# Performance work log

Measured on AMD Instinct MI355X. Metric: run time of the kernel, lower is better.

## Reference

```python
import jax, jax.numpy as jnp
import numpy as np

D_MODEL = 1024
H = 16
D_K = D_MODEL // H
WINDOW = 256
NEG = -1.0e9


def setup_inputs() -> dict:
    key = jax.random.key(0)
    ks = jax.random.split(key, 12)
    B, S = 1, 4096
    scale = 1.0 / np.sqrt(D_MODEL)
    inp = {
        'q': jax.random.normal(ks[0], (B, S, D_MODEL), dtype=jnp.float32),
        'k': jax.random.normal(ks[1], (B, S, D_MODEL), dtype=jnp.float32),
        'v': jax.random.normal(ks[2], (B, S, D_MODEL), dtype=jnp.float32),
        'w_q': jax.random.normal(ks[3], (D_MODEL, D_MODEL), dtype=jnp.float32) * scale,
        'b_q': jnp.zeros((D_MODEL,), dtype=jnp.float32),
        'w_k': jax.random.normal(ks[4], (D_MODEL, D_MODEL), dtype=jnp.float32) * scale,
        'b_k': jnp.zeros((D_MODEL,), dtype=jnp.float32),
        'w_v': jax.random.normal(ks[5], (D_MODEL, D_MODEL), dtype=jnp.float32) * scale,
        'b_v': jnp.zeros((D_MODEL,), dtype=jnp.float32),
        'w_o': jax.random.normal(ks[6], (D_MODEL, D_MODEL), dtype=jnp.float32) * scale,
        'b_o': jnp.zeros((D_MODEL,), dtype=jnp.float32),
    }
    return inp


def _local_mask(seq_len: int, window_size: int) -> jnp.ndarray:
    left = (window_size - 1) // 2
    right = window_size - 1 - left
    row = jnp.arange(seq_len)[:, None]
    col = jnp.arange(seq_len)[None, :]
    return (col >= row - left) & (col <= row + right)  # [S, S] bool


def reference(q, k, v, w_q, b_q, w_k, b_k, w_v, b_v, w_o, b_o):
    B, Sq, _ = q.shape
    Sk = k.shape[1]
    # projections (torch Linear: x @ W.T + b) -> [B, h, S, d_k]
    query = (q @ w_q.T + b_q).reshape(B, Sq, H, D_K).transpose(0, 2, 1, 3)
    key = (k @ w_k.T + b_k).reshape(B, Sk, H, D_K).transpose(0, 2, 1, 3)
    value = (v @ w_v.T + b_v).reshape(B, Sk, H, D_K).transpose(0, 2, 1, 3)

    scores = jnp.einsum('bhqd,bhkd->bhqk', query, key) / jnp.sqrt(
        jnp.asarray(D_K, dtype=query.dtype))
    if Sq == Sk:
        mask = _local_mask(Sq, WINDOW)  # [S, S]
        scores = jnp.where(mask[None, None], scores, jnp.asarray(NEG, scores.dtype))
    attn = jax.nn.softmax(scores, axis=-1)
    x = jnp.einsum('bhqk,bhkd->bhqd', attn, value)
    x = x.transpose(0, 2, 1, 3).reshape(B, Sq, D_MODEL)
    return x @ w_o.T + b_o
```

## Files before the change

kernel.cpp:

```cpp
#include <hip/hip_runtime.h>

#define SEQ 4096
#define DM 1024
#define NH 16
#define DK 64

typedef _Float16 half8 __attribute__((ext_vector_type(8)));
typedef _Float16 half4v __attribute__((ext_vector_type(4)));
typedef float f32x4 __attribute__((ext_vector_type(4)));

#define MFMA16(a, b, c) __builtin_amdgcn_mfma_f32_16x16x32_f16((a), (b), (c), 0, 0, 0)
#define GLOAD_LDS(g, l)                                                                  \
    __builtin_amdgcn_global_load_lds((const __attribute__((address_space(1))) void*)(g), \
                                     (__attribute__((address_space(3))) void*)(l), 16, 0, 0)

__device__ __forceinline__ float dpp_max16(float x) {
    x = fmaxf(x, __int_as_float(__builtin_amdgcn_update_dpp(
                     0, __float_as_int(x), 0xB1, 0xF, 0xF, true)));
    x = fmaxf(x, __int_as_float(__builtin_amdgcn_update_dpp(
                     0, __float_as_int(x), 0x4E, 0xF, 0xF, true)));
    x = fmaxf(x, __int_as_float(__builtin_amdgcn_update_dpp(
                     0, __float_as_int(x), 0x124, 0xF, 0xF, true)));
    x = fmaxf(x, __int_as_float(__builtin_amdgcn_update_dpp(
                     0, __float_as_int(x), 0x128, 0xF, 0xF, true)));
    return x;
}

__global__ void cvt_all(const float* __restrict__ q, const float* __restrict__ k,
                        const float* __restrict__ v, const float* __restrict__ wq,
                        const float* __restrict__ wk, const float* __restrict__ wv,
                        const float* __restrict__ wo, _Float16* __restrict__ qh,
                        _Float16* __restrict__ kh, _Float16* __restrict__ vh,
                        _Float16* __restrict__ wqh, _Float16* __restrict__ wkh,
                        _Float16* __restrict__ wvh, _Float16* __restrict__ woh) {
    int z = blockIdx.y;
    const float* src;
    _Float16* dst;
    int n;
    switch (z) {
    case 0: src = q;  dst = qh;  n = SEQ * DM; break;
    case 1: src = k;  dst = kh;  n = SEQ * DM; break;
    case 2: src = v;  dst = vh;  n = SEQ * DM; break;
    case 3: src = wq; dst = wqh; n = DM * DM;  break;
    case 4: src = wk; dst = wkh; n = DM * DM;  break;
    case 5: src = wv; dst = wvh; n = DM * DM;  break;
    default: src = wo; dst = woh; n = DM * DM; break;
    }
    int idx = (blockIdx.x * 256 + threadIdx.x) * 8;
    if (idx >= n) return;
    float4 f0 = *(const float4*)(src + idx);
    float4 f1 = *(const float4*)(src + idx + 4);
    half8 h;
    h[0] = (_Float16)f0.x; h[1] = (_Float16)f0.y; h[2] = (_Float16)f0.z; h[3] = (_Float16)f0.w;
    h[4] = (_Float16)f1.x; h[5] = (_Float16)f1.y; h[6] = (_Float16)f1.z; h[7] = (_Float16)f1.w;
    *(half8*)(dst + idx) = h;
}

template <int MT>
__device__ __forceinline__ void gemm_bk32_db(const _Float16* __restrict__ A,
                                             const _Float16* __restrict__ B, int m0, int n0,
                                             _Float16* As, _Float16* Bs, f32x4 (*acc)[4]) {
    constexpr int MI = MT / 32;
    constexpr int ACH = MT / 64;
    constexpr int ABUF = MT * 32;
    const int tid = threadIdx.x;
    const int wave = tid >> 6, lane = tid & 63;
    const int quad = lane >> 4, l16 = lane & 15;
    const int wr = (wave >> 1) * (MT / 2);
    const int wc = (wave & 1) * 64;
    const int srow = tid >> 2, scol = (tid & 3) * 8;

#pragma unroll
    for (int j = 0; j < ACH; ++j)
        GLOAD_LDS(A + (size_t)(m0 + j * 64 + srow) * DM + scol, As + j * 2048 + tid * 8);
#pragma unroll
    for (int j = 0; j < 2; ++j)
        GLOAD_LDS(B + (size_t)(n0 + j * 64 + srow) * DM + scol, Bs + j * 2048 + tid * 8);
    __syncthreads();

    int cur = 0;
    for (int k0 = 0; k0 < DM; k0 += 32) {
        const int nxt = cur ^ 1;
        if (k0 + 32 < DM) {
            int kc = k0 + 32 + scol;
#pragma unroll
            for (int j = 0; j < ACH; ++j)
                GLOAD_LDS(A + (size_t)(m0 + j * 64 + srow) * DM + kc,
                          As + nxt * ABUF + j * 2048 + tid * 8);
#pragma unroll
            for (int j = 0; j < 2; ++j)
                GLOAD_LDS(B + (size_t)(n0 + j * 64 + srow) * DM + kc,
                          Bs + nxt * 4096 + j * 2048 + tid * 8);
        }
        half8 af[MI], bf[4];
#pragma unroll
        for (int mi = 0; mi < MI; ++mi)
            af[mi] = *(const half8*)&As[cur * ABUF + (wr + mi * 16 + l16) * 32 + quad * 8];
#pragma unroll
        for (int ni = 0; ni < 4; ++ni)
            bf[ni] = *(const half8*)&Bs[cur * 4096 + (wc + ni * 16 + l16) * 32 + quad * 8];
#pragma unroll
        for (int mi = 0; mi < MI; ++mi)
#pragma unroll
            for (int ni = 0; ni < 4; ++ni)
                acc[mi][ni] = MFMA16(af[mi], bf[ni], acc[mi][ni]);
        __syncthreads();
        cur = nxt;
    }
}

__global__ void __launch_bounds__(256, 3) gemm_qkv(
    const _Float16* __restrict__ qh, const _Float16* __restrict__ kh,
    const _Float16* __restrict__ vh, const _Float16* __restrict__ wqh,
    const _Float16* __restrict__ wkh, const _Float16* __restrict__ wvh,
    const float* __restrict__ bq, const float* __restrict__ bk, const float* __restrict__ bv,
    _Float16* __restrict__ Qo, _Float16* __restrict__ Ko, _Float16* __restrict__ Vt) {
    __shared__ _Float16 As[2 * 128 * 32];
    __shared__ _Float16 Bs[2 * 128 * 32];
    int z = blockIdx.z;
    const _Float16 *A, *B;
    const float* bias;
    float scale;
    if (z == 0) { A = qh; B = wqh; bias = bq; scale = 0.125f; }
    else if (z == 1) { A = kh; B = wkh; bias = bk; scale = 1.0f; }
    else { A = vh; B = wvh; bias = bv; scale = 1.0f; }

    int m0 = blockIdx.x * 128;
    int n0 = blockIdx.y * 128;
    f32x4 acc[4][4] = {};
    gemm_bk32_db<128>(A, B, m0, n0, As, Bs, acc);

    const int tid = threadIdx.x;
    const int wave = tid >> 6, lane = tid & 63;
    const int quad = lane >> 4, l16 = lane & 15;
    const int wr = (wave >> 1) * 64;
    const int wc = (wave & 1) * 64;
    float bs[4];
#pragma unroll
    for (int ni = 0; ni < 4; ++ni) bs[ni] = bias[n0 + wc + ni * 16 + l16];

    if (z < 2) {
        _Float16* C = (z == 0) ? Qo : Ko;
#pragma unroll
        for (int mi = 0; mi < 4; ++mi)
#pragma unroll
            for (int ni = 0; ni < 4; ++ni) {
                int m = m0 + wr + mi * 16 + quad * 4;
                int n = n0 + wc + ni * 16 + l16;
#pragma unroll
                for (int r = 0; r < 4; ++r)
                    C[(size_t)(m + r) * DM + n] = (_Float16)((acc[mi][ni][r] + bs[ni]) * scale);
            }
    } else {
#pragma unroll
        for (int mi = 0; mi < 4; ++mi)
#pragma unroll
            for (int ni = 0; ni < 4; ++ni) {
                int m = m0 + wr + mi * 16 + quad * 4;
                int n = n0 + wc + ni * 16 + l16;
                half4v p;
#pragma unroll
                for (int r = 0; r < 4; ++r) p[r] = (_Float16)(acc[mi][ni][r] + bs[ni]);
                *(half4v*)(Vt + (size_t)n * SEQ + m) = p;
            }
    }
}

__global__ void __launch_bounds__(256, 3) gemm_out(const _Float16* __restrict__ Xh,
                                                   const _Float16* __restrict__ woh,
                                                   const float* __restrict__ bo,
                                                   float* __restrict__ out) {
    __shared__ _Float16 As[2 * 64 * 32];
    __shared__ _Float16 Bs[2 * 128 * 32];
    int m0 = blockIdx.x * 64;
    int n0 = blockIdx.y * 128;
    f32x4 acc[2][4] = {};
    gemm_bk32_db<64>(Xh, woh, m0, n0, As, Bs, acc);

    const int tid = threadIdx.x;
    const int wave = tid >> 6, lane = tid & 63;
    const int quad = lane >> 4, l16 = lane & 15;
    const int wr = (wave >> 1) * 32;
    const int wc = (wave & 1) * 64;
#pragma unroll
    for (int mi = 0; mi < 2; ++mi)
#pragma unroll
        for (int ni = 0; ni < 4; ++ni) {
            int m = m0 + wr + mi * 16 + quad * 4;
            int n = n0 + wc + ni * 16 + l16;
            float b = bo[n];
#pragma unroll
            for (int r = 0; r < 4; ++r) out[(size_t)(m + r) * DM + n] = acc[mi][ni][r] + b;
        }
}

__global__ void __launch_bounds__(256, 4) attn_kernel(const _Float16* __restrict__ Q,
                                                      const _Float16* __restrict__ K,
                                                      const _Float16* __restrict__ Vt,
                                                      _Float16* __restrict__ X) {
    __shared__ _Float16 Ks[320 * 64];
    __shared__ _Float16 Pl[4][16][40];
    int tid = threadIdx.x;
    int wave = tid >> 6, lane = tid & 63;
    int quad = lane >> 4, l16 = lane & 15;
    int h = blockIdx.y;
    int bx = ((blockIdx.x & 7) << 3) + (blockIdx.x >> 3);
    int q0b = bx * 64;
    int q0 = q0b + wave * 16;
    int kspan0 = q0b - 128;

    const _Float16* Kg = K + h * DK;
#pragma unroll
    for (int i = 0; i < 10; ++i) {
        int U = i * 256 + tid;
        int row = U >> 3, u = U & 7;
        int rg = kspan0 + row;
        rg = rg < 0 ? 0 : (rg > SEQ - 1 ? SEQ - 1 : rg);
        GLOAD_LDS(Kg + (size_t)rg * DM + ((u ^ (row & 7)) << 3), Ks + U * 8);
    }

    const _Float16* Qp = Q + (size_t)(q0 + l16) * DM + h * DK + quad * 8;
    half8 aq0 = *(const half8*)(Qp);
    half8 aq1 = *(const half8*)(Qp + 32);
    const half8 ones = {(_Float16)1, (_Float16)1, (_Float16)1, (_Float16)1,
                        (_Float16)1, (_Float16)1, (_Float16)1, (_Float16)1};

    float rowM[4], rowL[4];
    f32x4 o[4] = {};
#pragma unroll
    for (int r = 0; r < 4; ++r) { rowM[r] = -__builtin_inff(); rowL[r] = 0.f; }

    int kstart = (q0 > 127) ? ((q0 - 127) & ~31) : 0;
    int kend = q0 + 143;
    if (kend > SEQ - 1) kend = SEQ - 1;
    const int xk = l16 & 7;

    __syncthreads();

    for (int kt = kstart; kt <= kend; kt += 32) {
        int rel = kt - kspan0;
        half8 vb[4];
#pragma unroll
        for (int ni = 0; ni < 4; ++ni)
            vb[ni] = *(const half8*)(Vt + (size_t)(h * DK + ni * 16 + l16) * SEQ + kt + quad * 8);

        f32x4 s[2];
#pragma unroll
        for (int cf = 0; cf < 2; ++cf) {
            int rr = rel + cf * 16 + l16;
            half8 b0 = *(const half8*)&Ks[rr * 64 + ((quad ^ xk) << 3)];
            half8 b1 = *(const half8*)&Ks[rr * 64 + (((quad + 4) ^ xk) << 3)];
            f32x4 z = {};
            z = MFMA16(aq0, b0, z);
            z = MFMA16(aq1, b1, z);
            s[cf] = z;
        }
        const bool full = (kt >= q0 - 112) && (kt <= q0 + 97);
        float alpha[4];
#pragma unroll
        for (int r = 0; r < 4; ++r) {
            float x0 = s[0][r], x1 = s[1][r];
            if (!full) {
                int row = q0 + quad * 4 + r;
                int key0 = kt + l16, key1 = kt + 16 + l16;
                if (key0 < row - 127 || key0 > row + 128) x0 = -1e30f;
                if (key1 < row - 127 || key1 > row + 128) x1 = -1e30f;
            }
            float t = dpp_max16(fmaxf(x0, x1));
            float mnew = fmaxf(rowM[r], t);
            alpha[r] = __expf(rowM[r] - mnew);
            float p0 = __expf(x0 - mnew);
            float p1 = __expf(x1 - mnew);
            Pl[wave][quad * 4 + r][l16] = (_Float16)p0;
            Pl[wave][quad * 4 + r][l16 + 16] = (_Float16)p1;
            rowM[r] = mnew;
        }
        half8 ap = *(const half8*)&Pl[wave][l16][quad * 8];
        f32x4 ts = {};
        ts = MFMA16(ap, ones, ts);
#pragma unroll
        for (int r = 0; r < 4; ++r) rowL[r] = rowL[r] * alpha[r] + ts[r];
#pragma unroll
        for (int ni = 0; ni < 4; ++ni) {
#pragma unroll
            for (int r = 0; r < 4; ++r) o[ni][r] *= alpha[r];
            o[ni] = MFMA16(ap, vb[ni], o[ni]);
        }
    }

    float rinv[4];
#pragma unroll
    for (int r = 0; r < 4; ++r) rinv[r] = 1.0f / rowL[r];
#pragma unroll
    for (int ni = 0; ni < 4; ++ni) {
        int n = h * DK + ni * 16 + l16;
#pragma unroll
        for (int r = 0; r < 4; ++r) {
            int m = q0 + quad * 4 + r;
            X[(size_t)m * DM + n] = (_Float16)(o[ni][r] * rinv[r]);
        }
    }
}

extern "C" void kernel_launch(void* const* d_in, const int* in_sizes, int n_in, void* d_out,
                              int out_size, void* d_ws, size_t ws_size, hipStream_t stream) {
    const float* q  = (const float*)d_in[0];
    const float* k  = (const float*)d_in[1];
    const float* v  = (const float*)d_in[2];
    const float* wq = (const float*)d_in[3];
    const float* bq = (const float*)d_in[4];
    const float* wk = (const float*)d_in[5];
    const float* bk = (const float*)d_in[6];
    const float* wv = (const float*)d_in[7];
    const float* bv = (const float*)d_in[8];
    const float* wo = (const float*)d_in[9];
    const float* bo = (const float*)d_in[10];

    const size_t SZ_T = (size_t)SEQ * DM * sizeof(_Float16);
    const size_t SZ_W = (size_t)DM * DM * sizeof(_Float16);
    char* p = (char*)d_ws;
    _Float16* qh  = (_Float16*)(p);
    _Float16* kh  = (_Float16*)(p + SZ_T);
    _Float16* vh  = (_Float16*)(p + 2 * SZ_T);
    _Float16* wqh = (_Float16*)(p + 3 * SZ_T);
    _Float16* wkh = (_Float16*)(p + 3 * SZ_T + SZ_W);
    _Float16* wvh = (_Float16*)(p + 3 * SZ_T + 2 * SZ_W);
    _Float16* woh = (_Float16*)(p + 3 * SZ_T + 3 * SZ_W);
    _Float16* Qo  = (_Float16*)(p + 3 * SZ_T + 4 * SZ_W);
    _Float16* Ko  = (_Float16*)(p + 4 * SZ_T + 4 * SZ_W);
    _Float16* Vt  = (_Float16*)(p + 5 * SZ_T + 4 * SZ_W);
    _Float16* Xh  = qh;

    cvt_all<<<dim3(2048, 7), 256, 0, stream>>>(q, k, v, wq, wk, wv, wo, qh, kh, vh, wqh, wkh,
                                               wvh, woh);
    gemm_qkv<<<dim3(32, 8, 3), 256, 0, stream>>>(qh, kh, vh, wqh, wkh, wvh, bq, bk, bv, Qo, Ko,
                                                 Vt);
    attn_kernel<<<dim3(SEQ / 64, NH), 256, 0, stream>>>(Qo, Ko, Vt, Xh);
    gemm_out<<<dim3(64, 8), 256, 0, stream>>>(Xh, woh, bo, (float*)d_out);
}
```

Baseline: 205.0 us.

## Prefetch two K-stages ahead in GEMM using vmcnt-counted waits

Restructures the double-buffered GEMM mainloop so both LDS buffers are filled up front. Each iteration waits with a partial s_waitcnt vmcnt, so only the current stage's loads must land, then reads fragments to registers. After a second barrier it issues the loads for k+64 into the just-consumed buffer before running the MFMAs. This keeps one extra stage of global-to-LDS loads in flight and replaces __syncthreads with raw barriers. It relies on hand-counted vmcnt values and adds wasted wraparound loads in the last iterations.

```diff
diff --git a/kernel.cpp b/kernel.cpp
--- a/kernel.cpp
+++ b/kernel.cpp
@@ -57,9 +57,9 @@
 }
 
 template <int MT>
-__device__ __forceinline__ void gemm_bk32_db(const _Float16* __restrict__ A,
-                                             const _Float16* __restrict__ B, int m0, int n0,
-                                             _Float16* As, _Float16* Bs, f32x4 (*acc)[4]) {
+__device__ __forceinline__ void gemm_bk32_cnt(const _Float16* __restrict__ A,
+                                              const _Float16* __restrict__ B, int m0, int n0,
+                                              _Float16* As, _Float16* Bs, f32x4 (*acc)[4]) {
     constexpr int MI = MT / 32;
     constexpr int ACH = MT / 64;
     constexpr int ABUF = MT * 32;
@@ -71,41 +71,55 @@
     const int srow = tid >> 2, scol = (tid & 3) * 8;
 
 #pragma unroll
-    for (int j = 0; j < ACH; ++j)
-        GLOAD_LDS(A + (size_t)(m0 + j * 64 + srow) * DM + scol, As + j * 2048 + tid * 8);
-#pragma unroll
-    for (int j = 0; j < 2; ++j)
-        GLOAD_LDS(B + (size_t)(n0 + j * 64 + srow) * DM + scol, Bs + j * 2048 + tid * 8);
-    __syncthreads();
+    for (int s = 0; s < 2; ++s) {
+        int kc = s * 32 + scol;
+#pragma unroll
+        for (int j = 0; j < ACH; ++j)
+            GLOAD_LDS(A + (size_t)(m0 + j * 64 + srow) * DM + kc,
+                      As + s * ABUF + j * 2048 + tid * 8);
+#pragma unroll
+        for (int j = 0; j < 2; ++j)
+            GLOAD_LDS(B + (size_t)(n0 + j * 64 + srow) * DM + kc,
+                      Bs + s * 4096 + j * 2048 + tid * 8);
+    }
 
     int cur = 0;
     for (int k0 = 0; k0 < DM; k0 += 32) {
-        const int nxt = cur ^ 1;
-        if (k0 + 32 < DM) {
-            int kc = k0 + 32 + scol;
+        if constexpr (MT == 128) asm volatile("s_waitcnt vmcnt(4)" ::: "memory");
+        else                     asm volatile("s_waitcnt vmcnt(3)" ::: "memory");
+        asm volatile("s_barrier" ::: "memory");
+
+        half8 af[MI], bf[4];
+#pragma unroll
+        for (int mi = 0; mi < MI; ++mi)
+            af[mi] = *(const half8*)&As[cur * ABUF + (wr + mi * 16 + l16) * 32 + quad * 8];
+#pragma unroll
+        for (int ni = 0; ni < 4; ++ni)
+            bf[ni] = *(const half8*)&Bs[cur * 4096 + (wc + ni * 16 + l16) * 32 + quad * 8];
+
+        asm volatile("s_waitcnt lgkmcnt(0)" ::: "memory");
+        __builtin_amdgcn_sched_barrier(0);
+        asm volatile("s_barrier" ::: "memory");
+
+        {
+            int k2 = k0 + 64;
+            if (k2 >= DM) k2 = 0;
+            int kc = k2 + scol;
 #pragma unroll
             for (int j = 0; j < ACH; ++j)
                 GLOAD_LDS(A + (size_t)(m0 + j * 64 + srow) * DM + kc,
-                          As + nxt * ABUF + j * 2048 + tid * 8);
+                          As + cur * ABUF + j * 2048 + tid * 8);
 #pragma unroll
             for (int j = 0; j < 2; ++j)
                 GLOAD_LDS(B + (size_t)(n0 + j * 64 + srow) * DM + kc,
-                          Bs + nxt * 4096 + j * 2048 + tid * 8);
-        }
-        half8 af[MI], bf[4];
-#pragma unroll
-        for (int mi = 0; mi < MI; ++mi)
-            af[mi] = *(const half8*)&As[cur * ABUF + (wr + mi * 16 + l16) * 32 + quad * 8];
-#pragma unroll
-        for (int ni = 0; ni < 4; ++ni)
-            bf[ni] = *(const half8*)&Bs[cur * 4096 + (wc + ni * 16 + l16) * 32 + quad * 8];
+                          Bs + cur * 4096 + j * 2048 + tid * 8);
+        }
 #pragma unroll
         for (int mi = 0; mi < MI; ++mi)
 #pragma unroll
             for (int ni = 0; ni < 4; ++ni)
                 acc[mi][ni] = MFMA16(af[mi], bf[ni], acc[mi][ni]);
-        __syncthreads();
-        cur = nxt;
+        cur ^= 1;
     }
 }
 
@@ -128,7 +142,7 @@
     int m0 = blockIdx.x * 128;
     int n0 = blockIdx.y * 128;
     f32x4 acc[4][4] = {};
-    gemm_bk32_db<128>(A, B, m0, n0, As, Bs, acc);
+    gemm_bk32_cnt<128>(A, B, m0, n0, As, Bs, acc);
 
     const int tid = threadIdx.x;
     const int wave = tid >> 6, lane = tid & 63;
@@ -175,7 +189,7 @@
     int m0 = blockIdx.x * 64;
     int n0 = blockIdx.y * 128;
     f32x4 acc[2][4] = {};
-    gemm_bk32_db<64>(Xh, woh, m0, n0, As, Bs, acc);
+    gemm_bk32_cnt<64>(Xh, woh, m0, n0, As, Bs, acc);
 
     const int tid = threadIdx.x;
     const int wave = tid >> 6, lane = tid & 63;
```

After: 195.4 us. 4.7% less time.
